# Kernel tuning notes

Hardware: AMD Instinct MI355X
Metric: run time of the kernel (lower is better)

Reference implementation:

```python
import jax, jax.numpy as jnp
import numpy as np

N = 100000       # nodes
E = 1600000      # edges (avg degree 16)
D = 128          # features_dim = hidden_dim = out_dim
G = 3            # group_num
NUM = 50000      # nodes present in all time groups
ALPHA = 0.2      # LeakyReLU slope
W_SCALE = 0.05


def setup_inputs() -> dict:
    key = jax.random.key(0)
    ks = jax.random.split(key, 8)
    x = jax.random.normal(ks[0], (N, D), jnp.float32)
    edge_index = jax.random.randint(ks[1], (2, E), 0, N, dtype=jnp.int64)
    past = jax.random.normal(ks[2], (G - 1, NUM, D), jnp.float32)
    W1 = jax.random.normal(ks[3], (2 * D, D), jnp.float32) * W_SCALE
    W2 = jax.random.normal(ks[4], (2 * D, D), jnp.float32) * W_SCALE
    W0 = jax.random.normal(ks[5], (D, D), jnp.float32) * W_SCALE
    Wp = jax.random.normal(ks[6], (G - 1, D, D), jnp.float32) * W_SCALE
    W_T = jax.random.normal(ks[7], (2 * D, D), jnp.float32) * W_SCALE
    return {"x": x, "past": past, "W1": W1, "W2": W2, "W0": W0,
            "Wp": Wp, "W_T": W_T, "edge_index": edge_index, "num": NUM}


def reference(x, past, W1, W2, W0, Wp, W_T, edge_index, num):
    src, dst = edge_index[0], edge_index[1]
    n = x.shape[0]
    deg = jax.ops.segment_sum(jnp.ones(src.shape[0], x.dtype), dst, num_segments=n)
    deg = jnp.maximum(deg, 1.0)[:, None]

    def sage_layer(h, W):
        # mean-aggregate neighbors, concat with self, linear + ReLU
        agg = jax.ops.segment_sum(h[src], dst, num_segments=n) / deg
        return jax.nn.relu(jnp.concatenate([h, agg], axis=1) @ W)

    feat = sage_layer(x, W1)      # [N, D]
    feat = sage_layer(feat, W2)   # [N, D]

    # temporal mean aggregation (dropout is identity in eval mode)
    time_feat = (feat[:num] @ W0 + jnp.einsum('knd,kde->ne', past, Wp)) / G
    fused = jnp.concatenate([feat[:num], time_feat], axis=1) @ W_T  # [num, D]
    f = jax.nn.leaky_relu(fused, ALPHA)
    f = f / jnp.maximum(jnp.linalg.norm(f, axis=1, keepdims=True), 1e-12)
    return jnp.concatenate([f, feat[num:]], axis=0)  # [N, D]
```

## Files before the change

kernel.cpp:

```cpp
#include <hip/hip_runtime.h>

#define FD 128
#define CAP 64
#define BSH 8
#define MAXNB 512

typedef __attribute__((ext_vector_type(8))) short bf16x8;
typedef __attribute__((ext_vector_type(4))) float f32x4;

__device__ __forceinline__ float bflo(unsigned v) { return __uint_as_float(v << 16); }
__device__ __forceinline__ float bfhi(unsigned v) { return __uint_as_float(v & 0xffff0000u); }
__device__ __forceinline__ unsigned short f2b(float f) {
  unsigned u = __float_as_uint(f);
  return (unsigned short)((u + 0x7fffu + ((u >> 16) & 1u)) >> 16);
}
__device__ __forceinline__ unsigned pack2(float x, float y) {
  return (unsigned)f2b(x) | ((unsigned)f2b(y) << 16);
}

__global__ __launch_bounds__(256) void k_hist(const int* __restrict__ src,
                                              const int* __restrict__ dst,
                                              int* __restrict__ binCnt, int E, int n, int NB) {
  __shared__ int lh[MAXNB];
  for (int i = threadIdx.x; i < NB; i += 256) lh[i] = 0;
  __syncthreads();
  for (int e = blockIdx.x * 256 + threadIdx.x; e < E; e += gridDim.x * 256) {
    unsigned s = (unsigned)src[e], d = (unsigned)dst[e];
    if (s < (unsigned)n && d < (unsigned)n) atomicAdd(&lh[d >> BSH], 1);
  }
  __syncthreads();
  for (int i = threadIdx.x; i < NB; i += 256) {
    int c = lh[i];
    if (c) atomicAdd(&binCnt[i], c);
  }
}

__global__ __launch_bounds__(512) void k_scan(const int* __restrict__ binCnt,
                                              int* __restrict__ binStart,
                                              int* __restrict__ binCur, int NB) {
  __shared__ int buf[512];
  int t = threadIdx.x;
  int v0 = (t < NB) ? binCnt[t] : 0;
  buf[t] = v0;
  __syncthreads();
  for (int off = 1; off < 512; off <<= 1) {
    int v = (t >= off) ? buf[t - off] : 0;
    __syncthreads();
    buf[t] += v;
    __syncthreads();
  }
  if (t < NB) {
    int ex = buf[t] - v0;
    binStart[t] = ex;
    binCur[t] = ex;
  }
}

__global__ __launch_bounds__(256) void k_binscatter(const int* __restrict__ src,
                                                    const int* __restrict__ dst,
                                                    int* __restrict__ binCur,
                                                    uint2* __restrict__ binned, int E, int n, int NB) {
  __shared__ int lcnt[MAXNB], lbase[MAXNB];
  const int CH = 4096;
  int e0 = blockIdx.x * CH;
  for (int i = threadIdx.x; i < NB; i += 256) lcnt[i] = 0;
  __syncthreads();
  int se[16], de[16];
#pragma unroll
  for (int k = 0; k < 16; ++k) {
    int e = e0 + k * 256 + threadIdx.x;
    int ok = e < E;
    unsigned s = ok ? (unsigned)src[e] : 0u;
    unsigned d = ok ? (unsigned)dst[e] : 0u;
    ok = ok && s < (unsigned)n && d < (unsigned)n;
    se[k] = (int)s;
    de[k] = ok ? (int)d : -1;
    if (ok) atomicAdd(&lcnt[d >> BSH], 1);
  }
  __syncthreads();
  for (int i = threadIdx.x; i < NB; i += 256) {
    int c = lcnt[i];
    lbase[i] = c ? atomicAdd(&binCur[i], c) : 0;
    lcnt[i] = 0;
  }
  __syncthreads();
#pragma unroll
  for (int k = 0; k < 16; ++k) {
    if (de[k] >= 0) {
      int b = de[k] >> BSH;
      int p = lbase[b] + atomicAdd(&lcnt[b], 1);
      binned[p] = make_uint2((unsigned)se[k], (unsigned)de[k]);
    }
  }
}

__global__ __launch_bounds__(256) void k_bucket2(const uint2* __restrict__ binned,
                                                 const int* __restrict__ binStart,
                                                 const int* __restrict__ binCnt,
                                                 int* __restrict__ cnt,
                                                 int* __restrict__ idx, int n) {
  __shared__ int lcnt[256];
  int bin = blockIdx.x;
  int base = bin << BSH;
  lcnt[threadIdx.x] = 0;
  __syncthreads();
  int s0 = binStart[bin], c0 = binCnt[bin];
  for (int i = threadIdx.x; i < c0; i += 256) {
    uint2 pr = binned[s0 + i];
    int p = atomicAdd(&lcnt[pr.y & 255], 1);
    if (p < CAP) idx[(size_t)pr.y * CAP + p] = (int)pr.x;
  }
  __syncthreads();
  int d = base + threadIdx.x;
  if (d < n) cnt[d] = lcnt[threadIdx.x];
}

__global__ __launch_bounds__(256) void k_xcast(const float4* __restrict__ x,
                                               unsigned short* __restrict__ xb, int total4) {
  int i = blockIdx.x * 256 + threadIdx.x;
  if (i >= total4) return;
  float4 v = x[i];
  *(uint2*)&xb[(size_t)i * 4] = make_uint2(pack2(v.x, v.y), pack2(v.z, v.w));
}

__global__ __launch_bounds__(64) void k_wpack(const float* __restrict__ W,
                                              unsigned short* __restrict__ Wf, int KROWS) {
  int nkt = KROWS >> 5;
  int ct = blockIdx.x % 8, kt = blockIdx.x / 8;
  int lane = threadIdx.x;
  int m = lane & 15, q = lane >> 4;
  int nn = ct * 16 + m;
  int k0 = kt * 32 + q * 8;
  unsigned short tmp[8];
#pragma unroll
  for (int j = 0; j < 8; ++j) tmp[j] = f2b(W[(size_t)(k0 + j) * FD + nn]);
  unsigned short* dst = Wf + ((size_t)(ct * nkt + kt) * 64 + lane) * 8;
  *(uint4*)dst = *(uint4*)tmp;
}

__global__ __launch_bounds__(64) void k_wpack3(const float* __restrict__ W0,
                                               const float* __restrict__ WpA,
                                               const float* __restrict__ WpB,
                                               unsigned short* __restrict__ Wf) {
  int ct = blockIdx.x % 8, kt = blockIdx.x / 8;
  const float* src = kt < 4 ? W0 : (kt < 8 ? WpA : WpB);
  int ktl = kt & 3;
  int lane = threadIdx.x;
  int m = lane & 15, q = lane >> 4;
  int nn = ct * 16 + m;
  int k0 = ktl * 32 + q * 8;
  unsigned short tmp[8];
#pragma unroll
  for (int j = 0; j < 8; ++j) tmp[j] = f2b(src[(size_t)(k0 + j) * FD + nn]);
  unsigned short* dst = Wf + ((size_t)(ct * 12 + kt) * 64 + lane) * 8;
  *(uint4*)dst = *(uint4*)tmp;
}

template <int OUT_BF16>
__global__ __launch_bounds__(256) void k_sage(const unsigned* __restrict__ hb,
                                              const int* __restrict__ cnt,
                                              const int* __restrict__ idx,
                                              const unsigned short* __restrict__ Wf,
                                              float* __restrict__ outf,
                                              unsigned short* __restrict__ outb, int n) {
  __shared__ unsigned short sa[32][264];
  int tid = threadIdx.x;
  int lane = tid & 63, wv = tid >> 6;
  int rowBase = blockIdx.x * 32;

  for (int i = tid; i < 32 * 64; i += 256) {
    int r = i >> 6, cp = i & 63;
    int gr = rowBase + r;
    unsigned v = (gr < n) ? hb[(size_t)gr * 64 + cp] : 0u;
    *(unsigned*)&sa[r][cp * 2] = v;
  }

  int rbase = wv * 8;
  const int* ip = idx + (size_t)(rowBase + rbase) * CAP;
  int vidx[8];
  int c[8];
  int maxc = 0;
#pragma unroll
  for (int j = 0; j < 8; ++j) {
    int gr = rowBase + rbase + j;
    int cj = (gr < n) ? min(cnt[gr], CAP) : 0;
    cj = __builtin_amdgcn_readfirstlane(cj);
    c[j] = cj;
    maxc = max(maxc, cj);
    vidx[j] = ip[j * CAP + lane];
  }
  float ax[8], ay[8];
#pragma unroll
  for (int j = 0; j < 8; ++j) { ax[j] = 0.f; ay[j] = 0.f; }

  for (int e = 0; e < maxc; e += 2) {
    int e1 = min(e + 1, CAP - 1);
#pragma unroll
    for (int j = 0; j < 8; ++j) {
      int s0 = __builtin_amdgcn_readlane(vidx[j], e);
      int s1 = __builtin_amdgcn_readlane(vidx[j], e1);
      s0 = (e < c[j]) ? s0 : n;
      s1 = (e + 1 < c[j]) ? s1 : n;
      unsigned v0 = hb[(size_t)s0 * 64 + lane];
      unsigned v1 = hb[(size_t)s1 * 64 + lane];
      ax[j] += bflo(v0) + bflo(v1);
      ay[j] += bfhi(v0) + bfhi(v1);
    }
  }
#pragma unroll
  for (int j = 0; j < 8; ++j) {
    float inv = 1.0f / fmaxf((float)c[j], 1.0f);
    *(unsigned*)&sa[rbase + j][FD + lane * 2] = pack2(ax[j] * inv, ay[j] * inv);
  }
  __syncthreads();

  int m = lane & 15, q = lane >> 4;
  f32x4 z = {0.f, 0.f, 0.f, 0.f};
  f32x4 acc[2][2] = {{z, z}, {z, z}};
  int ct0 = wv * 2;
  const bf16x8* WfV = (const bf16x8*)Wf;
#pragma unroll
  for (int kt = 0; kt < 8; ++kt) {
    bf16x8 a0 = *(const bf16x8*)&sa[m][kt * 32 + q * 8];
    bf16x8 a1 = *(const bf16x8*)&sa[16 + m][kt * 32 + q * 8];
    bf16x8 b0 = WfV[(size_t)(ct0 * 8 + kt) * 64 + lane];
    bf16x8 b1 = WfV[(size_t)((ct0 + 1) * 8 + kt) * 64 + lane];
    acc[0][0] = __builtin_amdgcn_mfma_f32_16x16x32_bf16(a0, b0, acc[0][0], 0, 0, 0);
    acc[0][1] = __builtin_amdgcn_mfma_f32_16x16x32_bf16(a0, b1, acc[0][1], 0, 0, 0);
    acc[1][0] = __builtin_amdgcn_mfma_f32_16x16x32_bf16(a1, b0, acc[1][0], 0, 0, 0);
    acc[1][1] = __builtin_amdgcn_mfma_f32_16x16x32_bf16(a1, b1, acc[1][1], 0, 0, 0);
  }

#pragma unroll
  for (int rt = 0; rt < 2; ++rt) {
#pragma unroll
    for (int t = 0; t < 2; ++t) {
      int col = (ct0 + t) * 16 + m;
#pragma unroll
      for (int reg = 0; reg < 4; ++reg) {
        int gr = rowBase + rt * 16 + q * 4 + reg;
        if (gr < n) {
          float v = fmaxf(acc[rt][t][reg], 0.f);
          if (OUT_BF16)
            outb[(size_t)gr * FD + col] = f2b(v);
          else
            outf[(size_t)gr * FD + col] = v;
        }
      }
    }
  }
}

__global__ __launch_bounds__(256) void k_fuse(const float* __restrict__ feat2,
                                              const float* __restrict__ past,
                                              const unsigned short* __restrict__ Wcf,
                                              const unsigned short* __restrict__ Wtf,
                                              float* __restrict__ out, int num) {
  __shared__ unsigned short sa[32][392];
  __shared__ float so[32][132];
  int tid = threadIdx.x;
  int lane = tid & 63, wv = tid >> 6;
  int base = blockIdx.x * 32;

  for (int i = tid; i < 32 * 64; i += 256) {
    int r = i >> 6, cp = i & 63;
    int gr = base + r;
    float2 vf = {0.f, 0.f}, v0 = {0.f, 0.f}, v1 = {0.f, 0.f};
    if (gr < num) {
      vf = *(const float2*)&feat2[(size_t)gr * FD + cp * 2];
      v0 = *(const float2*)&past[(size_t)gr * FD + cp * 2];
      v1 = *(const float2*)&past[(size_t)num * FD + (size_t)gr * FD + cp * 2];
    }
    *(unsigned*)&sa[r][cp * 2]       = pack2(vf.x, vf.y);
    *(unsigned*)&sa[r][FD + cp * 2]  = pack2(v0.x, v0.y);
    *(unsigned*)&sa[r][256 + cp * 2] = pack2(v1.x, v1.y);
  }
  __syncthreads();

  int m = lane & 15, q = lane >> 4;
  int ct0 = wv * 2;
  f32x4 z = {0.f, 0.f, 0.f, 0.f};
  const bf16x8* WcV = (const bf16x8*)Wcf;
  const bf16x8* WtV = (const bf16x8*)Wtf;

  f32x4 acc[2][2] = {{z, z}, {z, z}};
#pragma unroll
  for (int kt = 0; kt < 12; ++kt) {
    bf16x8 a0 = *(const bf16x8*)&sa[m][kt * 32 + q * 8];
    bf16x8 a1 = *(const bf16x8*)&sa[16 + m][kt * 32 + q * 8];
    bf16x8 b0 = WcV[(size_t)(ct0 * 12 + kt) * 64 + lane];
    bf16x8 b1 = WcV[(size_t)((ct0 + 1) * 12 + kt) * 64 + lane];
    acc[0][0] = __builtin_amdgcn_mfma_f32_16x16x32_bf16(a0, b0, acc[0][0], 0, 0, 0);
    acc[0][1] = __builtin_amdgcn_mfma_f32_16x16x32_bf16(a0, b1, acc[0][1], 0, 0, 0);
    acc[1][0] = __builtin_amdgcn_mfma_f32_16x16x32_bf16(a1, b0, acc[1][0], 0, 0, 0);
    acc[1][1] = __builtin_amdgcn_mfma_f32_16x16x32_bf16(a1, b1, acc[1][1], 0, 0, 0);
  }
  __syncthreads();

  const float inv3 = 1.0f / 3.0f;
#pragma unroll
  for (int rt = 0; rt < 2; ++rt)
#pragma unroll
    for (int t = 0; t < 2; ++t) {
      int col = (ct0 + t) * 16 + m;
#pragma unroll
      for (int reg = 0; reg < 4; ++reg)
        sa[rt * 16 + q * 4 + reg][FD + col] = f2b(acc[rt][t][reg] * inv3);
    }
  __syncthreads();

  f32x4 acc2[2][2] = {{z, z}, {z, z}};
#pragma unroll
  for (int kt = 0; kt < 8; ++kt) {
    bf16x8 a0 = *(const bf16x8*)&sa[m][kt * 32 + q * 8];
    bf16x8 a1 = *(const bf16x8*)&sa[16 + m][kt * 32 + q * 8];
    bf16x8 b0 = WtV[(size_t)(ct0 * 8 + kt) * 64 + lane];
    bf16x8 b1 = WtV[(size_t)((ct0 + 1) * 8 + kt) * 64 + lane];
    acc2[0][0] = __builtin_amdgcn_mfma_f32_16x16x32_bf16(a0, b0, acc2[0][0], 0, 0, 0);
    acc2[0][1] = __builtin_amdgcn_mfma_f32_16x16x32_bf16(a0, b1, acc2[0][1], 0, 0, 0);
    acc2[1][0] = __builtin_amdgcn_mfma_f32_16x16x32_bf16(a1, b0, acc2[1][0], 0, 0, 0);
    acc2[1][1] = __builtin_amdgcn_mfma_f32_16x16x32_bf16(a1, b1, acc2[1][1], 0, 0, 0);
  }

#pragma unroll
  for (int rt = 0; rt < 2; ++rt)
#pragma unroll
    for (int t = 0; t < 2; ++t) {
      int col = (ct0 + t) * 16 + m;
#pragma unroll
      for (int reg = 0; reg < 4; ++reg) {
        float v = acc2[rt][t][reg];
        so[rt * 16 + q * 4 + reg][col] = v > 0.f ? v : 0.2f * v;
      }
    }
  __syncthreads();

#pragma unroll
  for (int j = 0; j < 8; ++j) {
    int r = wv * 8 + j;
    float v0 = so[r][lane * 2], v1 = so[r][lane * 2 + 1];
    float ss = v0 * v0 + v1 * v1;
#pragma unroll
    for (int mk = 32; mk >= 1; mk >>= 1) ss += __shfl_xor(ss, mk, 64);
    float inv = 1.0f / fmaxf(sqrtf(ss), 1e-12f);
    int gr = base + r;
    if (gr < num) {
      float2 o = {v0 * inv, v1 * inv};
      *(float2*)&out[(size_t)gr * FD + lane * 2] = o;
    }
  }
}

extern "C" void kernel_launch(void* const* d_in, const int* in_sizes, int n_in,
                              void* d_out, int out_size, void* d_ws, size_t ws_size,
                              hipStream_t stream) {
  const float* x    = (const float*)d_in[0];
  const float* past = (const float*)d_in[1];
  const float* W1   = (const float*)d_in[2];
  const float* W2   = (const float*)d_in[3];
  const float* W0   = (const float*)d_in[4];
  const float* Wp   = (const float*)d_in[5];
  const float* WT   = (const float*)d_in[6];
  const int*   ei   = (const int*)d_in[7];

  int N   = in_sizes[0] / FD;
  int NUM = in_sizes[1] / (2 * FD);
  int E   = in_sizes[7] / 2;
  const int* src = ei;
  const int* dst = ei + E;
  float* out = (float*)d_out;

  int NB = (N + 255) >> BSH;

  char* p = (char*)d_ws;
  int* cnt      = (int*)p;  p += (((size_t)N * 4 + 255) & ~(size_t)255);
  int* idx      = (int*)p;  p += (size_t)N * CAP * 4;
  int* binCnt   = (int*)p;  p += MAXNB * 4;
  int* binStart = (int*)p;  p += MAXNB * 4;
  int* binCur   = (int*)p;  p += MAXNB * 4;
  uint2* binned = (uint2*)p; p += (size_t)E * 8;
  unsigned short* xb  = (unsigned short*)p; p += (size_t)(N + 1) * FD * 2;
  unsigned short* f1b = (unsigned short*)p; p += (size_t)(N + 1) * FD * 2;
  unsigned short* w1f = (unsigned short*)p; p += (size_t)8 * 8 * 64 * 8 * 2;
  unsigned short* w2f = (unsigned short*)p; p += (size_t)8 * 8 * 64 * 8 * 2;
  unsigned short* wcf = (unsigned short*)p; p += (size_t)8 * 12 * 64 * 8 * 2;
  unsigned short* wtf = (unsigned short*)p;

  hipMemsetAsync(binCnt, 0, MAXNB * sizeof(int), stream);
  hipMemsetAsync(xb + (size_t)N * FD, 0, FD * 2, stream);
  hipMemsetAsync(f1b + (size_t)N * FD, 0, FD * 2, stream);

  k_hist<<<400, 256, 0, stream>>>(src, dst, binCnt, E, N, NB);
  k_scan<<<1, 512, 0, stream>>>(binCnt, binStart, binCur, NB);
  k_binscatter<<<(E + 4095) / 4096, 256, 0, stream>>>(src, dst, binCur, binned, E, N, NB);
  k_bucket2<<<NB, 256, 0, stream>>>(binned, binStart, binCnt, cnt, idx, N);

  k_xcast<<<(N * 32 + 255) / 256, 256, 0, stream>>>((const float4*)x, xb, N * 32);
  k_wpack<<<64, 64, 0, stream>>>(W1, w1f, 2 * FD);
  k_wpack<<<64, 64, 0, stream>>>(W2, w2f, 2 * FD);
  k_wpack3<<<96, 64, 0, stream>>>(W0, Wp, Wp + FD * FD, wcf);
  k_wpack<<<64, 64, 0, stream>>>(WT, wtf, 2 * FD);

  int sageGrid = (N + 31) / 32;
  k_sage<1><<<sageGrid, 256, 0, stream>>>((const unsigned*)xb, cnt, idx, w1f, nullptr, f1b, N);
  k_sage<0><<<sageGrid, 256, 0, stream>>>((const unsigned*)f1b, cnt, idx, w2f, out, nullptr, N);
  k_fuse<<<(NUM + 31) / 32, 256, 0, stream>>>(out, past, wcf, wtf, out, NUM);
}
```

Measured before the change: 407.5 us.

## Vectorize SAGE neighbor gather, merge weight-pack launches, pass bf16 feat to fuse

The neighbor-aggregation loop now uses 16-byte loads. Each quarter-wave fetches a different neighbor's full row, and partial sums are reduced across the quarters with cross-lane shuffles. This replaces the earlier one-neighbor-per-step 4-byte-per-lane gathers. The four weight-pack kernels and two memsets are merged into one prep launch that also zeroes the sentinel rows. Layer 2 writes bf16 output for the first num rows into the reused xb buffer, so k_fuse reads half the bytes, and launch bounds request occupancy 4. The trade is higher register pressure from the 64 accumulators and more shuffle work.

```diff
diff --git a/kernel.cpp b/kernel.cpp
--- a/kernel.cpp
+++ b/kernel.cpp
@@ -123,46 +123,55 @@
   *(uint2*)&xb[(size_t)i * 4] = make_uint2(pack2(v.x, v.y), pack2(v.z, v.w));
 }
 
-__global__ __launch_bounds__(64) void k_wpack(const float* __restrict__ W,
-                                              unsigned short* __restrict__ Wf, int KROWS) {
-  int nkt = KROWS >> 5;
-  int ct = blockIdx.x % 8, kt = blockIdx.x / 8;
+__global__ __launch_bounds__(64) void k_prep(const float* __restrict__ W1,
+                                             const float* __restrict__ W2,
+                                             const float* __restrict__ W0,
+                                             const float* __restrict__ WpA,
+                                             const float* __restrict__ WpB,
+                                             const float* __restrict__ WT,
+                                             unsigned short* __restrict__ w1f,
+                                             unsigned short* __restrict__ w2f,
+                                             unsigned short* __restrict__ wcf,
+                                             unsigned short* __restrict__ wtf,
+                                             unsigned* __restrict__ sent_x,
+                                             unsigned* __restrict__ sent_f) {
+  int b = blockIdx.x;
   int lane = threadIdx.x;
-  int m = lane & 15, q = lane >> 4;
-  int nn = ct * 16 + m;
-  int k0 = kt * 32 + q * 8;
-  unsigned short tmp[8];
-#pragma unroll
-  for (int j = 0; j < 8; ++j) tmp[j] = f2b(W[(size_t)(k0 + j) * FD + nn]);
-  unsigned short* dst = Wf + ((size_t)(ct * nkt + kt) * 64 + lane) * 8;
-  *(uint4*)dst = *(uint4*)tmp;
-}
-
-__global__ __launch_bounds__(64) void k_wpack3(const float* __restrict__ W0,
-                                               const float* __restrict__ WpA,
-                                               const float* __restrict__ WpB,
-                                               unsigned short* __restrict__ Wf) {
-  int ct = blockIdx.x % 8, kt = blockIdx.x / 8;
-  const float* src = kt < 4 ? W0 : (kt < 8 ? WpA : WpB);
-  int ktl = kt & 3;
-  int lane = threadIdx.x;
+  if (b >= 288) {
+    unsigned* d = (b == 288) ? sent_x : sent_f;
+    d[lane] = 0u;
+    return;
+  }
+  const float* srcW;
+  unsigned short* Wf;
+  int nkt, bb;
+  if (b < 64)       { srcW = W1; Wf = w1f; nkt = 8;  bb = b; }
+  else if (b < 128) { srcW = W2; Wf = w2f; nkt = 8;  bb = b - 64; }
+  else if (b < 224) { srcW = W0; Wf = wcf; nkt = 12; bb = b - 128; }
+  else              { srcW = WT; Wf = wtf; nkt = 8;  bb = b - 224; }
+  int ct = bb % 8, kt = bb / 8;
+  int ktl = kt;
+  if (nkt == 12) {
+    srcW = kt < 4 ? W0 : (kt < 8 ? WpA : WpB);
+    ktl = kt & 3;
+  }
   int m = lane & 15, q = lane >> 4;
   int nn = ct * 16 + m;
   int k0 = ktl * 32 + q * 8;
   unsigned short tmp[8];
 #pragma unroll
-  for (int j = 0; j < 8; ++j) tmp[j] = f2b(src[(size_t)(k0 + j) * FD + nn]);
-  unsigned short* dst = Wf + ((size_t)(ct * 12 + kt) * 64 + lane) * 8;
+  for (int j = 0; j < 8; ++j) tmp[j] = f2b(srcW[(size_t)(k0 + j) * FD + nn]);
+  unsigned short* dst = Wf + ((size_t)(ct * nkt + kt) * 64 + lane) * 8;
   *(uint4*)dst = *(uint4*)tmp;
 }
 
-template <int OUT_BF16>
-__global__ __launch_bounds__(256) void k_sage(const unsigned* __restrict__ hb,
-                                              const int* __restrict__ cnt,
-                                              const int* __restrict__ idx,
-                                              const unsigned short* __restrict__ Wf,
-                                              float* __restrict__ outf,
-                                              unsigned short* __restrict__ outb, int n) {
+__global__ __launch_bounds__(256, 4) void k_sage(const unsigned* __restrict__ hb,
+                                                 const int* __restrict__ cnt,
+                                                 const int* __restrict__ idx,
+                                                 const unsigned short* __restrict__ Wf,
+                                                 float* __restrict__ outf,
+                                                 unsigned short* __restrict__ outb,
+                                                 int n, int split) {
   __shared__ unsigned short sa[32][264];
   int tid = threadIdx.x;
   int lane = tid & 63, wv = tid >> 6;
@@ -177,8 +186,9 @@
 
   int rbase = wv * 8;
   const int* ip = idx + (size_t)(rowBase + rbase) * CAP;
-  int vidx[8];
-  int c[8];
+  int slot = lane >> 4;
+  int fq = lane & 15;
+  int vidx[8], c[8];
   int maxc = 0;
 #pragma unroll
   for (int j = 0; j < 8; ++j) {
@@ -187,30 +197,39 @@
     cj = __builtin_amdgcn_readfirstlane(cj);
     c[j] = cj;
     maxc = max(maxc, cj);
-    vidx[j] = ip[j * CAP + lane];
-  }
-  float ax[8], ay[8];
-#pragma unroll
-  for (int j = 0; j < 8; ++j) { ax[j] = 0.f; ay[j] = 0.f; }
-
-  for (int e = 0; e < maxc; e += 2) {
-    int e1 = min(e + 1, CAP - 1);
+    int vi = ip[j * CAP + lane];
+    vidx[j] = (lane < cj) ? vi : n;
+  }
+  float acc8[8][8];
+#pragma unroll
+  for (int j = 0; j < 8; ++j)
+#pragma unroll
+    for (int t = 0; t < 8; ++t) acc8[j][t] = 0.f;
+
+  for (int e0 = 0; e0 < maxc; e0 += 4) {
 #pragma unroll
     for (int j = 0; j < 8; ++j) {
-      int s0 = __builtin_amdgcn_readlane(vidx[j], e);
-      int s1 = __builtin_amdgcn_readlane(vidx[j], e1);
-      s0 = (e < c[j]) ? s0 : n;
-      s1 = (e + 1 < c[j]) ? s1 : n;
-      unsigned v0 = hb[(size_t)s0 * 64 + lane];
-      unsigned v1 = hb[(size_t)s1 * 64 + lane];
-      ax[j] += bflo(v0) + bflo(v1);
-      ay[j] += bfhi(v0) + bfhi(v1);
+      int s = __shfl(vidx[j], e0 + slot, 64);
+      uint4 v = *(const uint4*)&hb[(size_t)s * 64 + fq * 4];
+      acc8[j][0] += bflo(v.x); acc8[j][1] += bfhi(v.x);
+      acc8[j][2] += bflo(v.y); acc8[j][3] += bfhi(v.y);
+      acc8[j][4] += bflo(v.z); acc8[j][5] += bfhi(v.z);
+      acc8[j][6] += bflo(v.w); acc8[j][7] += bfhi(v.w);
     }
   }
 #pragma unroll
   for (int j = 0; j < 8; ++j) {
     float inv = 1.0f / fmaxf((float)c[j], 1.0f);
-    *(unsigned*)&sa[rbase + j][FD + lane * 2] = pack2(ax[j] * inv, ay[j] * inv);
+    unsigned o[4];
+#pragma unroll
+    for (int t = 0; t < 4; ++t) {
+      float a = acc8[j][2 * t], b = acc8[j][2 * t + 1];
+      a += __shfl_xor(a, 16, 64); b += __shfl_xor(b, 16, 64);
+      a += __shfl_xor(a, 32, 64); b += __shfl_xor(b, 32, 64);
+      o[t] = pack2(a * inv, b * inv);
+    }
+    if (slot == 0)
+      *(uint4*)&sa[rbase + j][FD + fq * 8] = make_uint4(o[0], o[1], o[2], o[3]);
   }
   __syncthreads();
 
@@ -241,7 +260,7 @@
         int gr = rowBase + rt * 16 + q * 4 + reg;
         if (gr < n) {
           float v = fmaxf(acc[rt][t][reg], 0.f);
-          if (OUT_BF16)
+          if (gr < split)
             outb[(size_t)gr * FD + col] = f2b(v);
           else
             outf[(size_t)gr * FD + col] = v;
@@ -251,7 +270,7 @@
   }
 }
 
-__global__ __launch_bounds__(256) void k_fuse(const float* __restrict__ feat2,
+__global__ __launch_bounds__(256) void k_fuse(const unsigned* __restrict__ f2b_in,
                                               const float* __restrict__ past,
                                               const unsigned short* __restrict__ Wcf,
                                               const unsigned short* __restrict__ Wtf,
@@ -265,13 +284,14 @@
   for (int i = tid; i < 32 * 64; i += 256) {
     int r = i >> 6, cp = i & 63;
     int gr = base + r;
-    float2 vf = {0.f, 0.f}, v0 = {0.f, 0.f}, v1 = {0.f, 0.f};
+    unsigned uf = 0;
+    float2 v0 = {0.f, 0.f}, v1 = {0.f, 0.f};
     if (gr < num) {
-      vf = *(const float2*)&feat2[(size_t)gr * FD + cp * 2];
+      uf = f2b_in[(size_t)gr * 64 + cp];
       v0 = *(const float2*)&past[(size_t)gr * FD + cp * 2];
       v1 = *(const float2*)&past[(size_t)num * FD + (size_t)gr * FD + cp * 2];
     }
-    *(unsigned*)&sa[r][cp * 2]       = pack2(vf.x, vf.y);
+    *(unsigned*)&sa[r][cp * 2]       = uf;
     *(unsigned*)&sa[r][FD + cp * 2]  = pack2(v0.x, v0.y);
     *(unsigned*)&sa[r][256 + cp * 2] = pack2(v1.x, v1.y);
   }
@@ -385,10 +405,9 @@
   unsigned short* w2f = (unsigned short*)p; p += (size_t)8 * 8 * 64 * 8 * 2;
   unsigned short* wcf = (unsigned short*)p; p += (size_t)8 * 12 * 64 * 8 * 2;
   unsigned short* wtf = (unsigned short*)p;
+  unsigned short* f2b_buf = xb;
 
   hipMemsetAsync(binCnt, 0, MAXNB * sizeof(int), stream);
-  hipMemsetAsync(xb + (size_t)N * FD, 0, FD * 2, stream);
-  hipMemsetAsync(f1b + (size_t)N * FD, 0, FD * 2, stream);
 
   k_hist<<<400, 256, 0, stream>>>(src, dst, binCnt, E, N, NB);
   k_scan<<<1, 512, 0, stream>>>(binCnt, binStart, binCur, NB);
@@ -396,13 +415,16 @@
   k_bucket2<<<NB, 256, 0, stream>>>(binned, binStart, binCnt, cnt, idx, N);
 
   k_xcast<<<(N * 32 + 255) / 256, 256, 0, stream>>>((const float4*)x, xb, N * 32);
-  k_wpack<<<64, 64, 0, stream>>>(W1, w1f, 2 * FD);
-  k_wpack<<<64, 64, 0, stream>>>(W2, w2f, 2 * FD);
-  k_wpack3<<<96, 64, 0, stream>>>(W0, Wp, Wp + FD * FD, wcf);
-  k_wpack<<<64, 64, 0, stream>>>(WT, wtf, 2 * FD);
+  k_prep<<<290, 64, 0, stream>>>(W1, W2, W0, Wp, Wp + FD * FD, WT,
+                                 w1f, w2f, wcf, wtf,
+                                 (unsigned*)(xb + (size_t)N * FD),
+                                 (unsigned*)(f1b + (size_t)N * FD));
 
   int sageGrid = (N + 31) / 32;
-  k_sage<1><<<sageGrid, 256, 0, stream>>>((const unsigned*)xb, cnt, idx, w1f, nullptr, f1b, N);
-  k_sage<0><<<sageGrid, 256, 0, stream>>>((const unsigned*)f1b, cnt, idx, w2f, out, nullptr, N);
-  k_fuse<<<(NUM + 31) / 32, 256, 0, stream>>>(out, past, wcf, wtf, out, NUM);
-}
+  k_sage<<<sageGrid, 256, 0, stream>>>((const unsigned*)xb, cnt, idx, w1f,
+                                       nullptr, f1b, N, N);
+  k_sage<<<sageGrid, 256, 0, stream>>>((const unsigned*)f1b, cnt, idx, w2f,
+                                       out, f2b_buf, N, NUM);
+  k_fuse<<<(NUM + 31) / 32, 256, 0, stream>>>((const unsigned*)f2b_buf, past,
+                                              wcf, wtf, out, NUM);
+}
```

Measured after the change: 457.0 us. 12.2% more time.
